# Performance work log

Measured on AMD Instinct MI355X. Metric: run time of the kernel, lower is better.

The kernel has to match this reference:

```python
import jax, jax.numpy as jnp
import numpy as np

N, E, D, O, M = 50000, 800000, 128, 128, 2

def _wn(x, v, g, b):
    # weight_norm linear: W = g * v / ||v||_row ; y = x @ W.T + b
    w = g * v / jnp.linalg.norm(v, axis=1, keepdims=True)
    return x @ w.T + b

def _gelu(x):
    return jax.nn.gelu(x, approximate=False)  # torch F.gelu default is exact erf

def setup_inputs() -> dict:
    key = jax.random.key(0)
    ks = jax.random.split(key, 32)
    inp = {"feat": jax.random.normal(ks[0], (N, D), jnp.float32)}
    layers = [("asrc", D, O), ("adst", D, O), ("asub", D, O), ("amul", D, O), ("aout", O, 1),
              ("pool", D, D), ("pool2", D, D), ("self", D, O), ("neigh", D, O), ("neigh2", D, O)]
    for i, (nm, fi, fo) in enumerate(layers):
        inp[nm + "_v"] = jax.random.normal(ks[i + 1], (fo, fi), jnp.float32) * (1.0 / np.sqrt(fi))
        inp[nm + "_g"] = jnp.ones((fo, 1), jnp.float32)
        inp[nm + "_b"] = jnp.zeros((fo,), jnp.float32)
    inp["mlp_v"] = jax.random.normal(ks[20], (M, O, O), jnp.float32) * (1.0 / np.sqrt(O))
    inp["mlp_g"] = jnp.ones((M, O, 1), jnp.float32)
    inp["mlp_b"] = jnp.zeros((M, O), jnp.float32)
    inp["src"] = jax.random.randint(ks[21], (E,), 0, N)
    inp["dst"] = jax.random.randint(ks[22], (E,), 0, N)
    return inp

def reference(feat, asrc_v, asrc_g, asrc_b, adst_v, adst_g, adst_b,
              asub_v, asub_g, asub_b, amul_v, amul_g, amul_b,
              aout_v, aout_g, aout_b, pool_v, pool_g, pool_b,
              pool2_v, pool2_g, pool2_b, self_v, self_g, self_b,
              neigh_v, neigh_g, neigh_b, neigh2_v, neigh2_g, neigh2_b,
              mlp_v, mlp_g, mlp_b, src, dst):
    fs, fd = feat[src], feat[dst]                        # [E, D] gathers
    e = (_wn(fs - fd, asub_v, asub_g, asub_b)
         + _wn(fs * fd, amul_v, amul_g, amul_b)
         + _wn(feat, asrc_v, asrc_g, asrc_b)[src]
         + _wn(feat, adst_v, adst_g, adst_b)[dst])       # [E, O]
    e = _gelu(e)
    e = jax.nn.leaky_relu(_wn(e, aout_v, aout_g, aout_b), 0.2)  # [E, 1] attention scalar

    cnt = jax.ops.segment_sum(jnp.ones((E,), feat.dtype), dst, num_segments=N)[:, None]  # in-degree

    h = _gelu(_wn(feat, pool_v, pool_g, pool_b))         # [N, D]
    neigh = jax.ops.segment_max(e * h[src], dst, num_segments=N)
    neigh = jnp.where(cnt > 0, neigh, jnp.zeros_like(neigh))  # zero for isolated dst nodes

    h2 = _gelu(_wn(feat, pool2_v, pool2_g, pool2_b))
    neigh2 = jax.ops.segment_sum(e * h2[src], dst, num_segments=N) / jnp.maximum(cnt, 1.0)

    rst = (_wn(feat, self_v, self_g, self_b)
           + _wn(neigh, neigh_v, neigh_g, neigh_b)
           + _wn(neigh2, neigh2_v, neigh2_g, neigh2_b))
    for i in range(M):
        rst = rst + _wn(_gelu(rst), mlp_v[i], mlp_g[i], mlp_b[i])
    return rst
```

## Files before the change

### kernel.cpp

```cpp
#include <hip/hip_runtime.h>
#include <hip/hip_bf16.h>
#include <math.h>

constexpr int NN = 50000;
constexpr int EE = 800000;

constexpr int OFF_WT_NODE  = 0;
constexpr int OFF_WT_AMUL  = 65536;
constexpr int OFF_WT_FINAL = 81920;
constexpr int OFF_WT_MLP   = 131072;
constexpr int OFF_WAOUT    = 163840;
constexpr int OFF_BE       = 163968;
constexpr int OFF_BFIN     = 164096;
constexpr int OFF_BAOUT    = 164224;
constexpr int OFF_WNODEBF  = 164240;
constexpr int OFF_WFINBF   = OFF_WNODEBF + 32768;
constexpr int OFF_WMLPBF   = OFF_WFINBF + 24576;
constexpr int OFF_WAMULBF  = OFF_WMLPBF + 16384;
constexpr int OFF_FEATBF   = OFF_WAMULBF + 8192;
constexpr int OFF_SBF      = OFF_FEATBF + NN*64;
constexpr int OFF_WEDGEBF  = OFF_SBF;
constexpr int OFF_HBF      = OFF_SBF + NN*128;
constexpr int OFF_SEV      = OFF_HBF + NN*128;
constexpr int OFF_NEIGHBF  = OFF_SEV + EE;
constexpr int OFF_STARTS   = OFF_NEIGHBF + NN*128;
constexpr int OFF_HIST     = OFF_STARTS + NN + 8;
constexpr int OFF_CURSOR   = OFF_HIST + NN;
constexpr int OFF_SSRCD    = OFF_CURSOR + NN;

constexpr int SCAN_NB = (NN + 255) / 256;

typedef __attribute__((ext_vector_type(8))) short bf16x8;
typedef __attribute__((ext_vector_type(4))) float f32x4;

__device__ __forceinline__ float gelu_f(float x) {
    float x2 = x * x;
    float w = x * fmaf(-0.1029448f, x2, -2.3022082f);
    return x * __builtin_amdgcn_rcpf(1.0f + __builtin_amdgcn_exp2f(w));
}
__device__ __forceinline__ float leaky_f(float x) {
    return x > 0.0f ? x : 0.2f * x;
}
__device__ __forceinline__ unsigned short f2bf(float x) {
    unsigned u = __float_as_uint(x);
    return (unsigned short)((u + 0x7fffu + ((u >> 16) & 1u)) >> 16);
}
__device__ __forceinline__ float bf2f(unsigned short b) {
    return __uint_as_float(((unsigned)b) << 16);
}
__device__ __forceinline__ unsigned pk_bf16(float lo, float hi) {
    __hip_bfloat16 l = __float2bfloat16(lo);
    __hip_bfloat16 h = __float2bfloat16(hi);
    unsigned short lu = *reinterpret_cast<unsigned short*>(&l);
    unsigned short hu = *reinterpret_cast<unsigned short*>(&h);
    return (unsigned)lu | ((unsigned)hu << 16);
}
__device__ __forceinline__ unsigned mulpack(unsigned a, unsigned b) {
    float a0 = __uint_as_float(a << 16), a1 = __uint_as_float(a & 0xffff0000u);
    float b0 = __uint_as_float(b << 16), b1 = __uint_as_float(b & 0xffff0000u);
    return pk_bf16(a0 * b0, a1 * b1);
}
__device__ __forceinline__ float block_sum128(float v, float* sbuf) {
    #pragma unroll
    for (int o = 32; o > 0; o >>= 1) v += __shfl_down(v, o, 64);
    int lane = threadIdx.x & 63, w = threadIdx.x >> 6;
    if (lane == 0) sbuf[w] = v;
    __syncthreads();
    float r = sbuf[0] + sbuf[1];
    __syncthreads();
    return r;
}

struct WnormArgs {
    const float *asrc_v, *asrc_g, *asrc_b;
    const float *adst_v, *adst_g, *adst_b;
    const float *asub_v, *asub_g, *asub_b;
    const float *amul_v, *amul_g, *amul_b;
    const float *aout_v, *aout_g, *aout_b;
    const float *pool_v, *pool_g, *pool_b;
    const float *pool2_v, *pool2_g, *pool2_b;
    const float *self_v, *self_g, *self_b;
    const float *neigh_v, *neigh_g, *neigh_b;
    const float *neigh2_v, *neigh2_g, *neigh2_b;
    const float *mlp_v, *mlp_g, *mlp_b;
    float* ws;
};

__global__ __launch_bounds__(128) void wnorm_kernel(WnormArgs a) {
    __shared__ float sbuf[2];
    int bid = blockIdx.x, i = threadIdx.x;
    float* ws = a.ws;
    if (bid < 1280) {
        int o = bid & 127, grp = bid >> 7;
        const float *v1 = nullptr, *g1 = nullptr, *v2 = nullptr, *g2 = nullptr;
        float sgn2 = 1.0f; float* dst = nullptr; int stride = 0;
        switch (grp) {
            case 0: v1=a.asrc_v; g1=a.asrc_g; v2=a.asub_v; g2=a.asub_g; sgn2= 1.f; dst=ws+OFF_WT_NODE+o;        stride=512; break;
            case 1: v1=a.adst_v; g1=a.adst_g; v2=a.asub_v; g2=a.asub_g; sgn2=-1.f; dst=ws+OFF_WT_NODE+128+o;    stride=512; break;
            case 2: v1=a.pool_v;  g1=a.pool_g;  dst=ws+OFF_WT_NODE+256+o;          stride=512; break;
            case 3: v1=a.pool2_v; g1=a.pool2_g; dst=ws+OFF_WT_NODE+384+o;          stride=512; break;
            case 4: v1=a.amul_v;  g1=a.amul_g;  dst=ws+OFF_WT_AMUL+o;              stride=128; break;
            case 5: v1=a.neigh_v; g1=a.neigh_g; dst=ws+OFF_WT_FINAL+o;             stride=128; break;
            case 6: v1=a.neigh2_v;g1=a.neigh2_g;dst=ws+OFF_WT_FINAL+128*128+o;     stride=128; break;
            case 7: v1=a.self_v;  g1=a.self_g;  dst=ws+OFF_WT_FINAL+256*128+o;     stride=128; break;
            case 8: v1=a.mlp_v;        g1=a.mlp_g;     dst=ws+OFF_WT_MLP+o;        stride=128; break;
            case 9: v1=a.mlp_v+16384;  g1=a.mlp_g+128; dst=ws+OFF_WT_MLP+16384+o;  stride=128; break;
        }
        float x1 = v1[o*128 + i];
        float n1 = sqrtf(block_sum128(x1*x1, sbuf));
        float w = g1[o] * x1 / n1;
        if (v2) {
            float x2 = v2[o*128 + i];
            float n2 = sqrtf(block_sum128(x2*x2, sbuf));
            w += sgn2 * g2[o] * x2 / n2;
        }
        dst[i * stride] = w;
    } else {
        float v = a.aout_v[i];
        float n = sqrtf(block_sum128(v*v, sbuf));
        ws[OFF_WAOUT + i] = a.aout_g[0] * v / n;
        ws[OFF_BE + i]    = a.asrc_b[i] + a.adst_b[i] + a.asub_b[i] + a.amul_b[i];
        ws[OFF_BFIN + i]  = a.self_b[i] + a.neigh_b[i] + a.neigh2_b[i];
        if (i == 0) ws[OFF_BAOUT] = a.aout_b[0];
    }
}

__global__ __launch_bounds__(256) void convert_weights_kernel(float* __restrict__ ws) {
    int idx = blockIdx.x * 256 + threadIdx.x;
    unsigned short* wnodebf = (unsigned short*)(ws + OFF_WNODEBF);
    unsigned short* wfinbf  = (unsigned short*)(ws + OFF_WFINBF);
    unsigned short* wmlpbf  = (unsigned short*)(ws + OFF_WMLPBF);
    unsigned short* wamulbf = (unsigned short*)(ws + OFF_WAMULBF);
    unsigned short* wedgebf = (unsigned short*)(ws + OFF_WEDGEBF);
    if (idx < 65536) {
        int k = idx >> 9, n = idx & 511;
        wnodebf[n * 128 + k] = f2bf(ws[OFF_WT_NODE + k * 512 + n]);
    } else if (idx < 114688) {
        int i = idx - 65536, k = i >> 7, o = i & 127;
        wfinbf[o * 384 + k] = f2bf(ws[OFF_WT_FINAL + k * 128 + o]);
    } else if (idx < 147456) {
        int i = idx - 114688, l = i >> 14, j = i & 16383, k = j >> 7, o = j & 127;
        wmlpbf[l * 16384 + o * 128 + k] = f2bf(ws[OFF_WT_MLP + l * 16384 + k * 128 + o]);
    } else if (idx < 163840) {
        int i = idx - 147456, k = i >> 7, o = i & 127;
        wamulbf[o * 128 + k] = f2bf(ws[OFF_WT_AMUL + k * 128 + o]);
    } else {
        int i = idx - 163840;
        int elem = i & 7, f = i >> 3;
        int lane = f & 63, kb = (f >> 6) & 3, ts = f >> 8;
        int t = ts / 3, slice = ts - t * 3;
        int o = t * 16 + (lane & 15);
        int kk = kb * 32 + (lane >> 4) * 8 + elem;
        float v = (slice == 0) ? ws[OFF_WT_AMUL + kk * 128 + o]
                : (slice == 1) ? ws[OFF_WT_NODE + kk * 512 + o]
                               : ws[OFF_WT_NODE + kk * 512 + 128 + o];
        wedgebf[i] = f2bf(v);
    }
}

__global__ __launch_bounds__(256) void hist_zero_kernel(float* __restrict__ ws) {
    int i = blockIdx.x * 256 + threadIdx.x;
    if (i < NN) ((int*)(ws + OFF_HIST))[i] = 0;
}

__global__ __launch_bounds__(256) void hist_kernel(const int* __restrict__ dst, float* __restrict__ ws) {
    int e = blockIdx.x * 256 + threadIdx.x;
    if (e < EE) atomicAdd(&((int*)(ws + OFF_HIST))[dst[e]], 1);
}

__global__ __launch_bounds__(256) void scan_blocks_kernel(float* __restrict__ ws) {
    __shared__ int wsum[4];
    const int* hist = (const int*)(ws + OFF_HIST);
    int* starts = (int*)(ws + OFF_STARTS);
    int* bsum = (int*)(ws + OFF_SEV);
    int bid = blockIdx.x, t = threadIdx.x;
    int idx = bid * 256 + t;
    int lane = t & 63, w = t >> 6;
    int v = (idx < NN) ? hist[idx] : 0;
    int s = v;
    #pragma unroll
    for (int o = 1; o < 64; o <<= 1) {
        int u = __shfl_up(s, o, 64);
        if (lane >= o) s += u;
    }
    if (lane == 63) wsum[w] = s;
    __syncthreads();
    int off = 0;
    for (int i = 0; i < w; ++i) off += wsum[i];
    int incl = s + off;
    if (idx < NN) starts[idx] = incl - v;
    if (t == 255) bsum[bid] = incl;
}

__global__ __launch_bounds__(256) void scan_tops_kernel(float* __restrict__ ws) {
    __shared__ int wsum[4];
    int* bsum = (int*)(ws + OFF_SEV);
    int t = threadIdx.x, lane = t & 63, w = t >> 6;
    int v = (t < SCAN_NB) ? bsum[t] : 0;
    int s = v;
    #pragma unroll
    for (int o = 1; o < 64; o <<= 1) {
        int u = __shfl_up(s, o, 64);
        if (lane >= o) s += u;
    }
    if (lane == 63) wsum[w] = s;
    __syncthreads();
    int off = 0;
    for (int i = 0; i < w; ++i) off += wsum[i];
    if (t < SCAN_NB) bsum[t] = s + off - v;
}

__global__ __launch_bounds__(256) void scan_add_kernel(float* __restrict__ ws) {
    int* starts = (int*)(ws + OFF_STARTS);
    int* cursor = (int*)(ws + OFF_CURSOR);
    const int* bsum = (const int*)(ws + OFF_SEV);
    int bid = blockIdx.x, t = threadIdx.x;
    int idx = bid * 256 + t;
    if (idx < NN) {
        int sv = starts[idx] + bsum[bid];
        starts[idx] = sv;
        cursor[idx] = sv;
    }
    if (idx == 0) starts[NN] = EE;
}

__global__ __launch_bounds__(256) void scatteridx_kernel(const int* __restrict__ src,
                                                         const int* __restrict__ dst,
                                                         float* __restrict__ ws) {
    int e = blockIdx.x * 256 + threadIdx.x;
    if (e >= EE) return;
    int d = dst[e];
    int pos = atomicAdd(&((int*)(ws + OFF_CURSOR))[d], 1);
    ((int2*)(ws + OFF_SSRCD))[pos] = make_int2(src[e], d);
}

__global__ __launch_bounds__(256) void segreduce_kernel(float* __restrict__ ws) {
    int n = blockIdx.x * 4 + (threadIdx.x >> 6);
    int lane = threadIdx.x & 63;
    const int* starts = (const int*)(ws + OFF_STARTS);
    const int2* ssrcd = (const int2*)(ws + OFF_SSRCD);
    const float* sev = ws + OFF_SEV;
    const unsigned short* hbf = (const unsigned short*)(ws + OFF_HBF);
    unsigned short* neighbf = (unsigned short*)(ws + OFF_NEIGHBF);
    int s0 = starts[n], s1 = starts[n + 1];
    float2 mx = make_float2(-INFINITY, -INFINITY);
    float2 sm = make_float2(0.f, 0.f);
    int i = s0;
    for (; i + 4 <= s1; i += 4) {
        int sA = ssrcd[i].x, sB = ssrcd[i + 1].x, sC = ssrcd[i + 2].x, sD = ssrcd[i + 3].x;
        float eA = sev[i], eB = sev[i + 1], eC = sev[i + 2], eD = sev[i + 3];
        unsigned hA = *(const unsigned*)&hbf[sA * 256 + lane * 2];
        unsigned gA = *(const unsigned*)&hbf[sA * 256 + 128 + lane * 2];
        unsigned hB = *(const unsigned*)&hbf[sB * 256 + lane * 2];
        unsigned gB = *(const unsigned*)&hbf[sB * 256 + 128 + lane * 2];
        unsigned hC = *(const unsigned*)&hbf[sC * 256 + lane * 2];
        unsigned gC = *(const unsigned*)&hbf[sC * 256 + 128 + lane * 2];
        unsigned hD = *(const unsigned*)&hbf[sD * 256 + lane * 2];
        unsigned gD = *(const unsigned*)&hbf[sD * 256 + 128 + lane * 2];
        mx.x = fmaxf(mx.x, eA * bf2f((unsigned short)(hA & 0xffffu)));
        mx.y = fmaxf(mx.y, eA * bf2f((unsigned short)(hA >> 16)));
        sm.x += eA * bf2f((unsigned short)(gA & 0xffffu));
        sm.y += eA * bf2f((unsigned short)(gA >> 16));
        mx.x = fmaxf(mx.x, eB * bf2f((unsigned short)(hB & 0xffffu)));
        mx.y = fmaxf(mx.y, eB * bf2f((unsigned short)(hB >> 16)));
        sm.x += eB * bf2f((unsigned short)(gB & 0xffffu));
        sm.y += eB * bf2f((unsigned short)(gB >> 16));
        mx.x = fmaxf(mx.x, eC * bf2f((unsigned short)(hC & 0xffffu)));
        mx.y = fmaxf(mx.y, eC * bf2f((unsigned short)(hC >> 16)));
        sm.x += eC * bf2f((unsigned short)(gC & 0xffffu));
        sm.y += eC * bf2f((unsigned short)(gC >> 16));
        mx.x = fmaxf(mx.x, eD * bf2f((unsigned short)(hD & 0xffffu)));
        mx.y = fmaxf(mx.y, eD * bf2f((unsigned short)(hD >> 16)));
        sm.x += eD * bf2f((unsigned short)(gD & 0xffffu));
        sm.y += eD * bf2f((unsigned short)(gD >> 16));
    }
    for (; i < s1; ++i) {
        int s = ssrcd[i].x;
        float ev = sev[i];
        unsigned hv  = *(const unsigned*)&hbf[s * 256 + lane * 2];
        unsigned h2v = *(const unsigned*)&hbf[s * 256 + 128 + lane * 2];
        mx.x = fmaxf(mx.x, ev * bf2f((unsigned short)(hv & 0xffffu)));
        mx.y = fmaxf(mx.y, ev * bf2f((unsigned short)(hv >> 16)));
        sm.x += ev * bf2f((unsigned short)(h2v & 0xffffu));
        sm.y += ev * bf2f((unsigned short)(h2v >> 16));
    }
    int cnt = s1 - s0;
    if (cnt == 0) { mx.x = 0.f; mx.y = 0.f; }
    float ic = 1.0f / (float)max(cnt, 1);
    *(unsigned*)&neighbf[n * 256 + lane * 2] = pk_bf16(mx.x, mx.y);
    *(unsigned*)&neighbf[n * 256 + 128 + lane * 2] = pk_bf16(sm.x * ic, sm.y * ic);
}

__global__ __launch_bounds__(256) void gemm_node_mfma(const float* __restrict__ feat,
                                                      const float* __restrict__ pool_b,
                                                      const float* __restrict__ pool2_b,
                                                      unsigned short* __restrict__ featbf,
                                                      unsigned short* __restrict__ hbf,
                                                      const unsigned short* __restrict__ wnodebf) {
    __shared__ unsigned short As[64 * 136];
    int tid = threadIdx.x;
    int row0 = blockIdx.x * 64;
    #pragma unroll
    for (int it = 0; it < 8; ++it) {
        int idx = tid + it * 256;
        int r = idx >> 5, u = idx & 31;
        int rr = min(row0 + r, NN - 1);
        float4 v = ((const float4*)feat)[rr * 32 + u];
        unsigned p0 = pk_bf16(v.x, v.y);
        unsigned p1 = pk_bf16(v.z, v.w);
        *(unsigned*)&As[r * 136 + u * 4]     = p0;
        *(unsigned*)&As[r * 136 + u * 4 + 2] = p1;
        *(uint2*)&featbf[rr * 128 + u * 4] = make_uint2(p0, p1);
    }
    __syncthreads();
    int lane = tid & 63, w = tid >> 6;
    int quad = lane >> 4, l15 = lane & 15;
    #pragma unroll 1
    for (int gy = 0; gy < 2; ++gy) {
        const unsigned short* B = wnodebf + (gy + 2) * 128 * 128;
        const float* bias = gy == 0 ? pool_b : pool2_b;
        f32x4 acc[8] = {};
        #pragma unroll 1
        for (int ks = 0; ks < 4; ++ks) {
            bf16x8 a = *(const bf16x8*)&As[(w * 16 + l15) * 136 + ks * 32 + quad * 8];
            #pragma unroll
            for (int t = 0; t < 8; ++t) {
                bf16x8 b = *(const bf16x8*)&B[(t * 16 + l15) * 128 + ks * 32 + quad * 8];
                acc[t] = __builtin_amdgcn_mfma_f32_16x16x32_bf16(a, b, acc[t], 0, 0, 0);
            }
        }
        #pragma unroll
        for (int reg = 0; reg < 4; ++reg) {
            int row = row0 + w * 16 + quad * 4 + reg;
            if (row >= NN) continue;
            #pragma unroll
            for (int t = 0; t < 8; ++t) {
                int col = t * 16 + l15;
                hbf[row * 256 + gy * 128 + col] = f2bf(gelu_f(acc[t][reg] + bias[col]));
            }
        }
    }
}

__global__ __launch_bounds__(256, 3) void gemm_edge(const unsigned short* __restrict__ featbf,
                                                    const unsigned short* __restrict__ wedgebf,
                                                    float* __restrict__ ws) {
    __shared__ unsigned short Bs[2][24 * 512];
    int tid = threadIdx.x;
    int lane = tid & 63, w = tid >> 6;
    int quad = lane >> 4, l15 = lane & 15;
    int e0 = blockIdx.x * 128;
    const int2* ssrcd = (const int2*)(ws + OFF_SSRCD);
    int base = e0 + w * 32 + l15;
    int2 i0 = ssrcd[base];
    int2 i1 = ssrcd[base + 16];
    const unsigned short* p0s = &featbf[i0.x * 128];
    const unsigned short* p0d = &featbf[i0.y * 128];
    const unsigned short* p1s = &featbf[i1.x * 128];
    const unsigned short* p1d = &featbf[i1.y * 128];
    int ko = quad * 8;

    uint4 ca[2][4];
    ca[0][0] = *(const uint4*)&p0s[ko];
    ca[0][1] = *(const uint4*)&p0d[ko];
    ca[0][2] = *(const uint4*)&p1s[ko];
    ca[0][3] = *(const uint4*)&p1d[ko];
    ca[1][0] = *(const uint4*)&p0s[ko + 32];
    ca[1][1] = *(const uint4*)&p0d[ko + 32];
    ca[1][2] = *(const uint4*)&p1s[ko + 32];
    ca[1][3] = *(const uint4*)&p1d[ko + 32];
    uint4 sb[6];
    #pragma unroll
    for (int i = 0; i < 6; ++i) {
        int ts = w * 6 + i;
        sb[i] = *(const uint4*)&wedgebf[(ts * 4 + 0) * 512 + lane * 8];
    }
    #pragma unroll
    for (int i = 0; i < 6; ++i) {
        int ts = w * 6 + i;
        *(uint4*)&Bs[0][ts * 512 + lane * 8] = sb[i];
    }
    __syncthreads();

    f32x4 acc0[8] = {}, acc1[8] = {};
    #pragma unroll
    for (int kb = 0; kb < 4; ++kb) {
        uint4 c0s = ca[kb & 1][0], c0d = ca[kb & 1][1];
        uint4 c1s = ca[kb & 1][2], c1d = ca[kb & 1][3];
        uint4 m0, m1;
        m0.x = mulpack(c0s.x, c0d.x); m0.y = mulpack(c0s.y, c0d.y);
        m0.z = mulpack(c0s.z, c0d.z); m0.w = mulpack(c0s.w, c0d.w);
        m1.x = mulpack(c1s.x, c1d.x); m1.y = mulpack(c1s.y, c1d.y);
        m1.z = mulpack(c1s.z, c1d.z); m1.w = mulpack(c1s.w, c1d.w);
        bf16x8 am0 = *(const bf16x8*)&m0,  am1 = *(const bf16x8*)&m1;
        bf16x8 as0 = *(const bf16x8*)&c0s, ad0 = *(const bf16x8*)&c0d;
        bf16x8 as1 = *(const bf16x8*)&c1s, ad1 = *(const bf16x8*)&c1d;
        if (kb < 2) {
            int k2 = ko + (kb + 2) * 32;
            ca[kb & 1][0] = *(const uint4*)&p0s[k2];
            ca[kb & 1][1] = *(const uint4*)&p0d[k2];
            ca[kb & 1][2] = *(const uint4*)&p1s[k2];
            ca[kb & 1][3] = *(const uint4*)&p1d[k2];
        }
        if (kb < 3) {
            #pragma unroll
            for (int i = 0; i < 6; ++i) {
                int ts = w * 6 + i;
                sb[i] = *(const uint4*)&wedgebf[(ts * 4 + kb + 1) * 512 + lane * 8];
            }
        }
        const unsigned short* bb = &Bs[kb & 1][lane * 8];
        #pragma unroll
        for (int t = 0; t < 8; ++t) {
            bf16x8 bm = *(const bf16x8*)&bb[(t * 3 + 0) * 512];
            bf16x8 b1 = *(const bf16x8*)&bb[(t * 3 + 1) * 512];
            bf16x8 b2 = *(const bf16x8*)&bb[(t * 3 + 2) * 512];
            acc0[t] = __builtin_amdgcn_mfma_f32_16x16x32_bf16(am0, bm, acc0[t], 0, 0, 0);
            acc1[t] = __builtin_amdgcn_mfma_f32_16x16x32_bf16(am1, bm, acc1[t], 0, 0, 0);
            acc0[t] = __builtin_amdgcn_mfma_f32_16x16x32_bf16(as0, b1, acc0[t], 0, 0, 0);
            acc1[t] = __builtin_amdgcn_mfma_f32_16x16x32_bf16(as1, b1, acc1[t], 0, 0, 0);
            acc0[t] = __builtin_amdgcn_mfma_f32_16x16x32_bf16(ad0, b2, acc0[t], 0, 0, 0);
            acc1[t] = __builtin_amdgcn_mfma_f32_16x16x32_bf16(ad1, b2, acc1[t], 0, 0, 0);
        }
        if (kb < 3) {
            #pragma unroll
            for (int i = 0; i < 6; ++i) {
                int ts = w * 6 + i;
                *(uint4*)&Bs[(kb + 1) & 1][ts * 512 + lane * 8] = sb[i];
            }
            __syncthreads();
        }
    }

    const float* waout = ws + OFF_WAOUT;
    const float* be = ws + OFF_BE;
    float b_aout = ws[OFF_BAOUT];
    float* e_out = ws + OFF_SEV;
    float wv[8], bv[8];
    #pragma unroll
    for (int t = 0; t < 8; ++t) { wv[t] = waout[t * 16 + l15]; bv[t] = be[t * 16 + l15]; }
    #pragma unroll
    for (int g = 0; g < 2; ++g) {
        #pragma unroll
        for (int reg = 0; reg < 4; ++reg) {
            int r = w * 32 + g * 16 + quad * 4 + reg;
            float partial = 0.0f;
            #pragma unroll
            for (int t = 0; t < 8; ++t) {
                float v = (g ? acc1[t][reg] : acc0[t][reg]) + bv[t];
                partial += gelu_f(v) * wv[t];
            }
            partial += __shfl_xor(partial, 1, 16);
            partial += __shfl_xor(partial, 2, 16);
            partial += __shfl_xor(partial, 4, 16);
            partial += __shfl_xor(partial, 8, 16);
            if (l15 == 0) e_out[e0 + r] = leaky_f(partial + b_aout);
        }
    }
}

__global__ __launch_bounds__(256) void gemm_final_mlp(const unsigned short* __restrict__ neighbf,
                                                      const unsigned short* __restrict__ featbf,
                                                      const unsigned short* __restrict__ wfinbf,
                                                      const unsigned short* __restrict__ wmlpbf,
                                                      const float* __restrict__ mlp_b,
                                                      float* __restrict__ out,
                                                      const float* __restrict__ ws) {
    __shared__ unsigned short As[64 * 392];
    __shared__ float bfin_s[128];
    int tid = threadIdx.x;
    int row0 = blockIdx.x * 64;
    if (tid < 128) bfin_s[tid] = ws[OFF_BFIN + tid];
    #pragma unroll
    for (int rg = 0; rg < 3; ++rg) {
        #pragma unroll
        for (int it = 0; it < 4; ++it) {
            int idx = tid + it * 256;
            int r = idx >> 4, u = idx & 15;
            int rr = min(row0 + r, NN - 1);
            const unsigned short* sp = (rg == 0) ? &neighbf[rr * 256 + u * 8]
                                     : (rg == 1) ? &neighbf[rr * 256 + 128 + u * 8]
                                                 : &featbf[rr * 128 + u * 8];
            *(uint4*)&As[r * 392 + rg * 128 + u * 8] = *(const uint4*)sp;
        }
    }
    __syncthreads();
    int lane = tid & 63, w = tid >> 6;
    int quad = lane >> 4, l15 = lane & 15;
    f32x4 rst[8] = {};
    #pragma unroll 1
    for (int ks = 0; ks < 12; ++ks) {
        bf16x8 a = *(const bf16x8*)&As[(w * 16 + l15) * 392 + ks * 32 + quad * 8];
        #pragma unroll
        for (int t = 0; t < 8; ++t) {
            bf16x8 b = *(const bf16x8*)&wfinbf[(t * 16 + l15) * 384 + ks * 32 + quad * 8];
            rst[t] = __builtin_amdgcn_mfma_f32_16x16x32_bf16(a, b, rst[t], 0, 0, 0);
        }
    }
    #pragma unroll
    for (int t = 0; t < 8; ++t) {
        float bf = bfin_s[t * 16 + l15];
        #pragma unroll
        for (int reg = 0; reg < 4; ++reg) rst[t][reg] += bf;
    }
    #pragma unroll 1
    for (int layer = 0; layer < 2; ++layer) {
        __syncthreads();
        #pragma unroll
        for (int t = 0; t < 8; ++t) {
            #pragma unroll
            for (int reg = 0; reg < 4; ++reg) {
                int row = w * 16 + quad * 4 + reg;
                As[row * 136 + t * 16 + l15] = f2bf(gelu_f(rst[t][reg]));
            }
        }
        __syncthreads();
        const unsigned short* wB = wmlpbf + layer * 16384;
        f32x4 acc[8] = {};
        #pragma unroll 1
        for (int ks = 0; ks < 4; ++ks) {
            bf16x8 a = *(const bf16x8*)&As[(w * 16 + l15) * 136 + ks * 32 + quad * 8];
            #pragma unroll
            for (int t = 0; t < 8; ++t) {
                bf16x8 b = *(const bf16x8*)&wB[(t * 16 + l15) * 128 + ks * 32 + quad * 8];
                acc[t] = __builtin_amdgcn_mfma_f32_16x16x32_bf16(a, b, acc[t], 0, 0, 0);
            }
        }
        #pragma unroll
        for (int t = 0; t < 8; ++t) {
            float bias = mlp_b[layer * 128 + t * 16 + l15];
            #pragma unroll
            for (int reg = 0; reg < 4; ++reg) rst[t][reg] += acc[t][reg] + bias;
        }
    }
    #pragma unroll
    for (int reg = 0; reg < 4; ++reg) {
        int row = row0 + w * 16 + quad * 4 + reg;
        if (row >= NN) continue;
        #pragma unroll
        for (int t = 0; t < 8; ++t) {
            out[row * 128 + t * 16 + l15] = rst[t][reg];
        }
    }
}

extern "C" void kernel_launch(void* const* d_in, const int* in_sizes, int n_in,
                              void* d_out, int out_size, void* d_ws, size_t ws_size,
                              hipStream_t stream) {
    const float* feat = (const float*)d_in[0];
    WnormArgs wa;
    wa.asrc_v = (const float*)d_in[1];  wa.asrc_g = (const float*)d_in[2];  wa.asrc_b = (const float*)d_in[3];
    wa.adst_v = (const float*)d_in[4];  wa.adst_g = (const float*)d_in[5];  wa.adst_b = (const float*)d_in[6];
    wa.asub_v = (const float*)d_in[7];  wa.asub_g = (const float*)d_in[8];  wa.asub_b = (const float*)d_in[9];
    wa.amul_v = (const float*)d_in[10]; wa.amul_g = (const float*)d_in[11]; wa.amul_b = (const float*)d_in[12];
    wa.aout_v = (const float*)d_in[13]; wa.aout_g = (const float*)d_in[14]; wa.aout_b = (const float*)d_in[15];
    wa.pool_v = (const float*)d_in[16]; wa.pool_g = (const float*)d_in[17]; wa.pool_b = (const float*)d_in[18];
    wa.pool2_v= (const float*)d_in[19]; wa.pool2_g= (const float*)d_in[20]; wa.pool2_b= (const float*)d_in[21];
    wa.self_v = (const float*)d_in[22]; wa.self_g = (const float*)d_in[23]; wa.self_b = (const float*)d_in[24];
    wa.neigh_v= (const float*)d_in[25]; wa.neigh_g= (const float*)d_in[26]; wa.neigh_b= (const float*)d_in[27];
    wa.neigh2_v=(const float*)d_in[28]; wa.neigh2_g=(const float*)d_in[29]; wa.neigh2_b=(const float*)d_in[30];
    wa.mlp_v  = (const float*)d_in[31]; wa.mlp_g  = (const float*)d_in[32]; wa.mlp_b  = (const float*)d_in[33];
    const int* src = (const int*)d_in[34];
    const int* dst = (const int*)d_in[35];
    float* out = (float*)d_out;
    float* ws = (float*)d_ws;
    wa.ws = ws;
    unsigned short* featbf  = (unsigned short*)(ws + OFF_FEATBF);
    unsigned short* hbf     = (unsigned short*)(ws + OFF_HBF);
    unsigned short* neighbf = (unsigned short*)(ws + OFF_NEIGHBF);
    unsigned short* wnodebf = (unsigned short*)(ws + OFF_WNODEBF);
    unsigned short* wfinbf  = (unsigned short*)(ws + OFF_WFINBF);
    unsigned short* wmlpbf  = (unsigned short*)(ws + OFF_WMLPBF);
    unsigned short* wedgebf = (unsigned short*)(ws + OFF_WEDGEBF);

    wnorm_kernel<<<dim3(1281), dim3(128), 0, stream>>>(wa);
    convert_weights_kernel<<<dim3(832), dim3(256), 0, stream>>>(ws);
    hist_zero_kernel<<<dim3((NN + 255) / 256), dim3(256), 0, stream>>>(ws);
    hist_kernel<<<dim3((EE + 255) / 256), dim3(256), 0, stream>>>(dst, ws);
    scan_blocks_kernel<<<dim3(SCAN_NB), dim3(256), 0, stream>>>(ws);
    scan_tops_kernel<<<dim3(1), dim3(256), 0, stream>>>(ws);
    scan_add_kernel<<<dim3(SCAN_NB), dim3(256), 0, stream>>>(ws);
    scatteridx_kernel<<<dim3((EE + 255) / 256), dim3(256), 0, stream>>>(src, dst, ws);
    gemm_node_mfma<<<dim3(782), dim3(256), 0, stream>>>(feat, wa.pool_b, wa.pool2_b, featbf, hbf, wnodebf);
    gemm_edge<<<dim3(EE / 128), dim3(256), 0, stream>>>(featbf, wedgebf, ws);
    segreduce_kernel<<<dim3(NN / 4), dim3(256), 0, stream>>>(ws);
    gemm_final_mlp<<<dim3(782), dim3(256), 0, stream>>>(neighbf, featbf, wfinbf, wmlpbf, wa.mlp_b, out, ws);
}
```

Baseline: 510.3 us.

## Switch MFMA path to fp16, interleave h/h2 layout, fold hist zeroing into wnorm

Replaces bf16 with fp16 for all staged activations and weights, using f16 MFMA instructions and packed f16 multiplies for the edge product in place of unpack/multiply/repack. Interleaves the h and h2 node features so segreduce fetches both with a single 8-byte load per source node. Moves histogram zeroing into the weight-norm kernel and drops the unused amul bf16 conversion, removing one launch and some conversion work. fp16 has a narrower range than bf16, so large activations could overflow.

```diff
diff --git a/kernel.cpp b/kernel.cpp
--- a/kernel.cpp
+++ b/kernel.cpp
@@ -30,7 +30,9 @@
 
 constexpr int SCAN_NB = (NN + 255) / 256;
 
-typedef __attribute__((ext_vector_type(8))) short bf16x8;
+typedef __attribute__((ext_vector_type(8))) _Float16 f16x8;
+typedef __attribute__((ext_vector_type(2))) _Float16 f16x2;
+typedef __attribute__((ext_vector_type(2))) __fp16 fp16x2r;
 typedef __attribute__((ext_vector_type(4))) float f32x4;
 
 __device__ __forceinline__ float gelu_f(float x) {
@@ -41,24 +43,23 @@
 __device__ __forceinline__ float leaky_f(float x) {
     return x > 0.0f ? x : 0.2f * x;
 }
-__device__ __forceinline__ unsigned short f2bf(float x) {
-    unsigned u = __float_as_uint(x);
-    return (unsigned short)((u + 0x7fffu + ((u >> 16) & 1u)) >> 16);
-}
-__device__ __forceinline__ float bf2f(unsigned short b) {
-    return __uint_as_float(((unsigned)b) << 16);
-}
-__device__ __forceinline__ unsigned pk_bf16(float lo, float hi) {
-    __hip_bfloat16 l = __float2bfloat16(lo);
-    __hip_bfloat16 h = __float2bfloat16(hi);
-    unsigned short lu = *reinterpret_cast<unsigned short*>(&l);
-    unsigned short hu = *reinterpret_cast<unsigned short*>(&h);
-    return (unsigned)lu | ((unsigned)hu << 16);
-}
-__device__ __forceinline__ unsigned mulpack(unsigned a, unsigned b) {
-    float a0 = __uint_as_float(a << 16), a1 = __uint_as_float(a & 0xffff0000u);
-    float b0 = __uint_as_float(b << 16), b1 = __uint_as_float(b & 0xffff0000u);
-    return pk_bf16(a0 * b0, a1 * b1);
+__device__ __forceinline__ unsigned pk_f16(float lo, float hi) {
+    fp16x2r p = __builtin_amdgcn_cvt_pkrtz(lo, hi);
+    return *reinterpret_cast<unsigned*>(&p);
+}
+__device__ __forceinline__ unsigned short f2h(float x) {
+    fp16x2r p = __builtin_amdgcn_cvt_pkrtz(x, 0.0f);
+    return *reinterpret_cast<unsigned short*>(&p);
+}
+__device__ __forceinline__ unsigned mulpack_h(unsigned a, unsigned b) {
+    f16x2 x = *reinterpret_cast<f16x2*>(&a);
+    f16x2 y = *reinterpret_cast<f16x2*>(&b);
+    f16x2 r = x * y;
+    return *reinterpret_cast<unsigned*>(&r);
+}
+__device__ __forceinline__ float2 up2(unsigned u) {
+    f16x2 p = *reinterpret_cast<f16x2*>(&u);
+    return make_float2((float)p.x, (float)p.y);
 }
 __device__ __forceinline__ float block_sum128(float v, float* sbuf) {
     #pragma unroll
@@ -90,6 +91,8 @@
     __shared__ float sbuf[2];
     int bid = blockIdx.x, i = threadIdx.x;
     float* ws = a.ws;
+    int gid = bid * 128 + i;
+    if (gid < NN) ((int*)(ws + OFF_HIST))[gid] = 0;
     if (bid < 1280) {
         int o = bid & 127, grp = bid >> 7;
         const float *v1 = nullptr, *g1 = nullptr, *v2 = nullptr, *g2 = nullptr;
@@ -130,22 +133,18 @@
     unsigned short* wnodebf = (unsigned short*)(ws + OFF_WNODEBF);
     unsigned short* wfinbf  = (unsigned short*)(ws + OFF_WFINBF);
     unsigned short* wmlpbf  = (unsigned short*)(ws + OFF_WMLPBF);
-    unsigned short* wamulbf = (unsigned short*)(ws + OFF_WAMULBF);
     unsigned short* wedgebf = (unsigned short*)(ws + OFF_WEDGEBF);
     if (idx < 65536) {
         int k = idx >> 9, n = idx & 511;
-        wnodebf[n * 128 + k] = f2bf(ws[OFF_WT_NODE + k * 512 + n]);
+        wnodebf[n * 128 + k] = f2h(ws[OFF_WT_NODE + k * 512 + n]);
     } else if (idx < 114688) {
         int i = idx - 65536, k = i >> 7, o = i & 127;
-        wfinbf[o * 384 + k] = f2bf(ws[OFF_WT_FINAL + k * 128 + o]);
+        wfinbf[o * 384 + k] = f2h(ws[OFF_WT_FINAL + k * 128 + o]);
     } else if (idx < 147456) {
         int i = idx - 114688, l = i >> 14, j = i & 16383, k = j >> 7, o = j & 127;
-        wmlpbf[l * 16384 + o * 128 + k] = f2bf(ws[OFF_WT_MLP + l * 16384 + k * 128 + o]);
-    } else if (idx < 163840) {
-        int i = idx - 147456, k = i >> 7, o = i & 127;
-        wamulbf[o * 128 + k] = f2bf(ws[OFF_WT_AMUL + k * 128 + o]);
+        wmlpbf[l * 16384 + o * 128 + k] = f2h(ws[OFF_WT_MLP + l * 16384 + k * 128 + o]);
     } else {
-        int i = idx - 163840;
+        int i = idx - 147456;
         int elem = i & 7, f = i >> 3;
         int lane = f & 63, kb = (f >> 6) & 3, ts = f >> 8;
         int t = ts / 3, slice = ts - t * 3;
@@ -154,13 +153,8 @@
         float v = (slice == 0) ? ws[OFF_WT_AMUL + kk * 128 + o]
                 : (slice == 1) ? ws[OFF_WT_NODE + kk * 512 + o]
                                : ws[OFF_WT_NODE + kk * 512 + 128 + o];
-        wedgebf[i] = f2bf(v);
-    }
-}
-
-__global__ __launch_bounds__(256) void hist_zero_kernel(float* __restrict__ ws) {
-    int i = blockIdx.x * 256 + threadIdx.x;
-    if (i < NN) ((int*)(ws + OFF_HIST))[i] = 0;
+        wedgebf[i] = f2h(v);
+    }
 }
 
 __global__ __launch_bounds__(256) void hist_kernel(const int* __restrict__ dst, float* __restrict__ ws) {
@@ -249,46 +243,36 @@
     for (; i + 4 <= s1; i += 4) {
         int sA = ssrcd[i].x, sB = ssrcd[i + 1].x, sC = ssrcd[i + 2].x, sD = ssrcd[i + 3].x;
         float eA = sev[i], eB = sev[i + 1], eC = sev[i + 2], eD = sev[i + 3];
-        unsigned hA = *(const unsigned*)&hbf[sA * 256 + lane * 2];
-        unsigned gA = *(const unsigned*)&hbf[sA * 256 + 128 + lane * 2];
-        unsigned hB = *(const unsigned*)&hbf[sB * 256 + lane * 2];
-        unsigned gB = *(const unsigned*)&hbf[sB * 256 + 128 + lane * 2];
-        unsigned hC = *(const unsigned*)&hbf[sC * 256 + lane * 2];
-        unsigned gC = *(const unsigned*)&hbf[sC * 256 + 128 + lane * 2];
-        unsigned hD = *(const unsigned*)&hbf[sD * 256 + lane * 2];
-        unsigned gD = *(const unsigned*)&hbf[sD * 256 + 128 + lane * 2];
-        mx.x = fmaxf(mx.x, eA * bf2f((unsigned short)(hA & 0xffffu)));
-        mx.y = fmaxf(mx.y, eA * bf2f((unsigned short)(hA >> 16)));
-        sm.x += eA * bf2f((unsigned short)(gA & 0xffffu));
-        sm.y += eA * bf2f((unsigned short)(gA >> 16));
-        mx.x = fmaxf(mx.x, eB * bf2f((unsigned short)(hB & 0xffffu)));
-        mx.y = fmaxf(mx.y, eB * bf2f((unsigned short)(hB >> 16)));
-        sm.x += eB * bf2f((unsigned short)(gB & 0xffffu));
-        sm.y += eB * bf2f((unsigned short)(gB >> 16));
-        mx.x = fmaxf(mx.x, eC * bf2f((unsigned short)(hC & 0xffffu)));
-        mx.y = fmaxf(mx.y, eC * bf2f((unsigned short)(hC >> 16)));
-        sm.x += eC * bf2f((unsigned short)(gC & 0xffffu));
-        sm.y += eC * bf2f((unsigned short)(gC >> 16));
-        mx.x = fmaxf(mx.x, eD * bf2f((unsigned short)(hD & 0xffffu)));
-        mx.y = fmaxf(mx.y, eD * bf2f((unsigned short)(hD >> 16)));
-        sm.x += eD * bf2f((unsigned short)(gD & 0xffffu));
-        sm.y += eD * bf2f((unsigned short)(gD >> 16));
+        uint2 vA = *(const uint2*)&hbf[sA * 256 + lane * 4];
+        uint2 vB = *(const uint2*)&hbf[sB * 256 + lane * 4];
+        uint2 vC = *(const uint2*)&hbf[sC * 256 + lane * 4];
+        uint2 vD = *(const uint2*)&hbf[sD * 256 + lane * 4];
+        float2 hA = up2(vA.x), gA = up2(vA.y);
+        float2 hB = up2(vB.x), gB = up2(vB.y);
+        float2 hC = up2(vC.x), gC = up2(vC.y);
+        float2 hD = up2(vD.x), gD = up2(vD.y);
+        mx.x = fmaxf(mx.x, eA * hA.x); mx.y = fmaxf(mx.y, eA * hA.y);
+        sm.x += eA * gA.x;             sm.y += eA * gA.y;
+        mx.x = fmaxf(mx.x, eB * hB.x); mx.y = fmaxf(mx.y, eB * hB.y);
+        sm.x += eB * gB.x;             sm.y += eB * gB.y;
+        mx.x = fmaxf(mx.x, eC * hC.x); mx.y = fmaxf(mx.y, eC * hC.y);
+        sm.x += eC * gC.x;             sm.y += eC * gC.y;
+        mx.x = fmaxf(mx.x, eD * hD.x); mx.y = fmaxf(mx.y, eD * hD.y);
+        sm.x += eD * gD.x;             sm.y += eD * gD.y;
     }
     for (; i < s1; ++i) {
         int s = ssrcd[i].x;
         float ev = sev[i];
-        unsigned hv  = *(const unsigned*)&hbf[s * 256 + lane * 2];
-        unsigned h2v = *(const unsigned*)&hbf[s * 256 + 128 + lane * 2];
-        mx.x = fmaxf(mx.x, ev * bf2f((unsigned short)(hv & 0xffffu)));
-        mx.y = fmaxf(mx.y, ev * bf2f((unsigned short)(hv >> 16)));
-        sm.x += ev * bf2f((unsigned short)(h2v & 0xffffu));
-        sm.y += ev * bf2f((unsigned short)(h2v >> 16));
+        uint2 v = *(const uint2*)&hbf[s * 256 + lane * 4];
+        float2 h = up2(v.x), g = up2(v.y);
+        mx.x = fmaxf(mx.x, ev * h.x); mx.y = fmaxf(mx.y, ev * h.y);
+        sm.x += ev * g.x;             sm.y += ev * g.y;
     }
     int cnt = s1 - s0;
     if (cnt == 0) { mx.x = 0.f; mx.y = 0.f; }
     float ic = 1.0f / (float)max(cnt, 1);
-    *(unsigned*)&neighbf[n * 256 + lane * 2] = pk_bf16(mx.x, mx.y);
-    *(unsigned*)&neighbf[n * 256 + 128 + lane * 2] = pk_bf16(sm.x * ic, sm.y * ic);
+    *(unsigned*)&neighbf[n * 256 + lane * 2] = pk_f16(mx.x, mx.y);
+    *(unsigned*)&neighbf[n * 256 + 128 + lane * 2] = pk_f16(sm.x * ic, sm.y * ic);
 }
 
 __global__ __launch_bounds__(256) void gemm_node_mfma(const float* __restrict__ feat,
@@ -306,8 +290,8 @@
         int r = idx >> 5, u = idx & 31;
         int rr = min(row0 + r, NN - 1);
         float4 v = ((const float4*)feat)[rr * 32 + u];
-        unsigned p0 = pk_bf16(v.x, v.y);
-        unsigned p1 = pk_bf16(v.z, v.w);
+        unsigned p0 = pk_f16(v.x, v.y);
+        unsigned p1 = pk_f16(v.z, v.w);
         *(unsigned*)&As[r * 136 + u * 4]     = p0;
         *(unsigned*)&As[r * 136 + u * 4 + 2] = p1;
         *(uint2*)&featbf[rr * 128 + u * 4] = make_uint2(p0, p1);
@@ -322,11 +306,11 @@
         f32x4 acc[8] = {};
         #pragma unroll 1
         for (int ks = 0; ks < 4; ++ks) {
-            bf16x8 a = *(const bf16x8*)&As[(w * 16 + l15) * 136 + ks * 32 + quad * 8];
+            f16x8 a = *(const f16x8*)&As[(w * 16 + l15) * 136 + ks * 32 + quad * 8];
             #pragma unroll
             for (int t = 0; t < 8; ++t) {
-                bf16x8 b = *(const bf16x8*)&B[(t * 16 + l15) * 128 + ks * 32 + quad * 8];
-                acc[t] = __builtin_amdgcn_mfma_f32_16x16x32_bf16(a, b, acc[t], 0, 0, 0);
+                f16x8 b = *(const f16x8*)&B[(t * 16 + l15) * 128 + ks * 32 + quad * 8];
+                acc[t] = __builtin_amdgcn_mfma_f32_16x16x32_f16(a, b, acc[t], 0, 0, 0);
             }
         }
         #pragma unroll
@@ -336,7 +320,8 @@
             #pragma unroll
             for (int t = 0; t < 8; ++t) {
                 int col = t * 16 + l15;
-                hbf[row * 256 + gy * 128 + col] = f2bf(gelu_f(acc[t][reg] + bias[col]));
+                hbf[row * 256 + ((col >> 1) << 2) + (col & 1) + gy * 2] =
+                    f2h(gelu_f(acc[t][reg] + bias[col]));
             }
         }
     }
@@ -388,13 +373,13 @@
         uint4 c0s = ca[kb & 1][0], c0d = ca[kb & 1][1];
         uint4 c1s = ca[kb & 1][2], c1d = ca[kb & 1][3];
         uint4 m0, m1;
-        m0.x = mulpack(c0s.x, c0d.x); m0.y = mulpack(c0s.y, c0d.y);
-        m0.z = mulpack(c0s.z, c0d.z); m0.w = mulpack(c0s.w, c0d.w);
-        m1.x = mulpack(c1s.x, c1d.x); m1.y = mulpack(c1s.y, c1d.y);
-        m1.z = mulpack(c1s.z, c1d.z); m1.w = mulpack(c1s.w, c1d.w);
-        bf16x8 am0 = *(const bf16x8*)&m0,  am1 = *(const bf16x8*)&m1;
-        bf16x8 as0 = *(const bf16x8*)&c0s, ad0 = *(const bf16x8*)&c0d;
-        bf16x8 as1 = *(const bf16x8*)&c1s, ad1 = *(const bf16x8*)&c1d;
+        m0.x = mulpack_h(c0s.x, c0d.x); m0.y = mulpack_h(c0s.y, c0d.y);
+        m0.z = mulpack_h(c0s.z, c0d.z); m0.w = mulpack_h(c0s.w, c0d.w);
+        m1.x = mulpack_h(c1s.x, c1d.x); m1.y = mulpack_h(c1s.y, c1d.y);
+        m1.z = mulpack_h(c1s.z, c1d.z); m1.w = mulpack_h(c1s.w, c1d.w);
+        f16x8 am0 = *(const f16x8*)&m0,  am1 = *(const f16x8*)&m1;
+        f16x8 as0 = *(const f16x8*)&c0s, ad0 = *(const f16x8*)&c0d;
+        f16x8 as1 = *(const f16x8*)&c1s, ad1 = *(const f16x8*)&c1d;
         if (kb < 2) {
             int k2 = ko + (kb + 2) * 32;
             ca[kb & 1][0] = *(const uint4*)&p0s[k2];
@@ -412,15 +397,15 @@
         const unsigned short* bb = &Bs[kb & 1][lane * 8];
         #pragma unroll
         for (int t = 0; t < 8; ++t) {
-            bf16x8 bm = *(const bf16x8*)&bb[(t * 3 + 0) * 512];
-            bf16x8 b1 = *(const bf16x8*)&bb[(t * 3 + 1) * 512];
-            bf16x8 b2 = *(const bf16x8*)&bb[(t * 3 + 2) * 512];
-            acc0[t] = __builtin_amdgcn_mfma_f32_16x16x32_bf16(am0, bm, acc0[t], 0, 0, 0);
-            acc1[t] = __builtin_amdgcn_mfma_f32_16x16x32_bf16(am1, bm, acc1[t], 0, 0, 0);
-            acc0[t] = __builtin_amdgcn_mfma_f32_16x16x32_bf16(as0, b1, acc0[t], 0, 0, 0);
-            acc1[t] = __builtin_amdgcn_mfma_f32_16x16x32_bf16(as1, b1, acc1[t], 0, 0, 0);
-            acc0[t] = __builtin_amdgcn_mfma_f32_16x16x32_bf16(ad0, b2, acc0[t], 0, 0, 0);
-            acc1[t] = __builtin_amdgcn_mfma_f32_16x16x32_bf16(ad1, b2, acc1[t], 0, 0, 0);
+            f16x8 bm = *(const f16x8*)&bb[(t * 3 + 0) * 512];
+            f16x8 b1 = *(const f16x8*)&bb[(t * 3 + 1) * 512];
+            f16x8 b2 = *(const f16x8*)&bb[(t * 3 + 2) * 512];
+            acc0[t] = __builtin_amdgcn_mfma_f32_16x16x32_f16(am0, bm, acc0[t], 0, 0, 0);
+            acc1[t] = __builtin_amdgcn_mfma_f32_16x16x32_f16(am1, bm, acc1[t], 0, 0, 0);
+            acc0[t] = __builtin_amdgcn_mfma_f32_16x16x32_f16(as0, b1, acc0[t], 0, 0, 0);
+            acc1[t] = __builtin_amdgcn_mfma_f32_16x16x32_f16(as1, b1, acc1[t], 0, 0, 0);
+            acc0[t] = __builtin_amdgcn_mfma_f32_16x16x32_f16(ad0, b2, acc0[t], 0, 0, 0);
+            acc1[t] = __builtin_amdgcn_mfma_f32_16x16x32_f16(ad1, b2, acc1[t], 0, 0, 0);
         }
         if (kb < 3) {
             #pragma unroll
@@ -490,11 +475,11 @@
     f32x4 rst[8] = {};
     #pragma unroll 1
     for (int ks = 0; ks < 12; ++ks) {
-        bf16x8 a = *(const bf16x8*)&As[(w * 16 + l15) * 392 + ks * 32 + quad * 8];
+        f16x8 a = *(const f16x8*)&As[(w * 16 + l15) * 392 + ks * 32 + quad * 8];
         #pragma unroll
         for (int t = 0; t < 8; ++t) {
-            bf16x8 b = *(const bf16x8*)&wfinbf[(t * 16 + l15) * 384 + ks * 32 + quad * 8];
-            rst[t] = __builtin_amdgcn_mfma_f32_16x16x32_bf16(a, b, rst[t], 0, 0, 0);
+            f16x8 b = *(const f16x8*)&wfinbf[(t * 16 + l15) * 384 + ks * 32 + quad * 8];
+            rst[t] = __builtin_amdgcn_mfma_f32_16x16x32_f16(a, b, rst[t], 0, 0, 0);
         }
     }
     #pragma unroll
@@ -511,7 +496,7 @@
             #pragma unroll
             for (int reg = 0; reg < 4; ++reg) {
                 int row = w * 16 + quad * 4 + reg;
-                As[row * 136 + t * 16 + l15] = f2bf(gelu_f(rst[t][reg]));
+                As[row * 136 + t * 16 + l15] = f2h(gelu_f(rst[t][reg]));
             }
         }
         __syncthreads();
@@ -519,11 +504,11 @@
         f32x4 acc[8] = {};
         #pragma unroll 1
         for (int ks = 0; ks < 4; ++ks) {
-            bf16x8 a = *(const bf16x8*)&As[(w * 16 + l15) * 136 + ks * 32 + quad * 8];
+            f16x8 a = *(const f16x8*)&As[(w * 16 + l15) * 136 + ks * 32 + quad * 8];
             #pragma unroll
             for (int t = 0; t < 8; ++t) {
-                bf16x8 b = *(const bf16x8*)&wB[(t * 16 + l15) * 128 + ks * 32 + quad * 8];
-                acc[t] = __builtin_amdgcn_mfma_f32_16x16x32_bf16(a, b, acc[t], 0, 0, 0);
+                f16x8 b = *(const f16x8*)&wB[(t * 16 + l15) * 128 + ks * 32 + quad * 8];
+                acc[t] = __builtin_amdgcn_mfma_f32_16x16x32_f16(a, b, acc[t], 0, 0, 0);
             }
         }
         #pragma unroll
@@ -574,8 +559,7 @@
     unsigned short* wedgebf = (unsigned short*)(ws + OFF_WEDGEBF);
 
     wnorm_kernel<<<dim3(1281), dim3(128), 0, stream>>>(wa);
-    convert_weights_kernel<<<dim3(832), dim3(256), 0, stream>>>(ws);
-    hist_zero_kernel<<<dim3((NN + 255) / 256), dim3(256), 0, stream>>>(ws);
+    convert_weights_kernel<<<dim3(768), dim3(256), 0, stream>>>(ws);
     hist_kernel<<<dim3((EE + 255) / 256), dim3(256), 0, stream>>>(dst, ws);
     scan_blocks_kernel<<<dim3(SCAN_NB), dim3(256), 0, stream>>>(ws);
     scan_tops_kernel<<<dim3(1), dim3(256), 0, stream>>>(ws);
```

After: 522.1 us. 2.3% more time.
